# Performance work log

Hardware: AMD Instinct MI355X
Metric: run time of the kernel (lower is better)

Reference implementation:

```python
import jax, jax.numpy as jnp
import numpy as np

P, LMAX, D, H = 4096, 64, 512, 512
NEG = -1e30


def setup_inputs() -> dict:
    key = jax.random.key(0)
    ks = jax.random.split(key, 8)
    paths_nodes = jax.random.normal(ks[0], (P, LMAX, D), dtype=jnp.float32)
    lengths = jax.random.randint(ks[1], (P,), 1, LMAX + 1, dtype=jnp.int32)
    s = 0.05
    return {
        "paths_nodes": paths_nodes,
        "lengths": lengths,
        "pW1": jax.random.normal(ks[2], (D, H), dtype=jnp.float32) * s,
        "pb1": jnp.zeros((H,), dtype=jnp.float32),
        "pw2": jax.random.normal(ks[3], (H,), dtype=jnp.float32) * s,
        "pb2": jnp.zeros((1,), dtype=jnp.float32),
        "aW1": jax.random.normal(ks[4], (D, H), dtype=jnp.float32) * s,
        "ab1": jnp.zeros((H,), dtype=jnp.float32),
        "aw2": jax.random.normal(ks[5], (H,), dtype=jnp.float32) * s,
        "ab2": jnp.zeros((1,), dtype=jnp.float32),
    }


def reference(paths_nodes, lengths, pW1, pb1, pw2, pb2, aW1, ab1, aw2, ab2):
    # paths_nodes: [P, L, D], lengths: [P]
    mask = jnp.arange(LMAX)[None, :] < lengths[:, None]  # [P, L] valid positions

    # per-path node attention: Linear -> ReLU -> Linear(->1), softmax over length
    h = jax.nn.relu(jnp.einsum('pld,dh->plh', paths_nodes, pW1) + pb1)  # [P,L,H]
    scores = jnp.einsum('plh,h->pl', h, pw2) + pb2[0]                   # [P,L]
    scores = jnp.where(mask, scores, NEG)
    w = jax.nn.softmax(scores, axis=1)                                  # [P,L]
    paths_fea = jnp.einsum('pl,pld->pd', w, paths_nodes)                # [P,D]

    # path-level attention: same MLP over path features, softmax over paths
    h2 = jax.nn.relu(paths_fea @ aW1 + ab1)                             # [P,H]
    a = h2 @ aw2 + ab2[0]                                               # [P]
    aw = jax.nn.softmax(a, axis=0)                                      # [P]
    user_fea = jnp.einsum('p,pd->d', aw, paths_fea)                     # [D]
    return user_fea
```

## Files before the change

### kernel.cpp

```cpp
#include <hip/hip_runtime.h>

typedef __attribute__((ext_vector_type(8))) short bf16x8;
typedef __attribute__((ext_vector_type(8))) unsigned short u16x8;
typedef __attribute__((ext_vector_type(4))) float f32x4;

__device__ __forceinline__ ushort f2bf(float x) {
  unsigned u = __float_as_uint(x);
  unsigned r = (u + 0x7fffu + ((u >> 16) & 1u)) >> 16;
  return (ushort)r;
}

typedef const __attribute__((address_space(1))) unsigned int ga_uint;
typedef __attribute__((address_space(3))) unsigned int lds_uint;
__device__ __forceinline__ void gload_lds16(const ushort* g, ushort* l) {
  __builtin_amdgcn_global_load_lds((ga_uint*)g, (lds_uint*)l, 16, 0, 0);
}

__global__ void transpose_convert(const float* __restrict__ w1, const float* __restrict__ w2,
                                  ushort* __restrict__ o1, ushort* __restrict__ o2) {
  __shared__ float tile[64][65];
  const float* src = (blockIdx.z == 0) ? w1 : w2;
  ushort* dst = (blockIdx.z == 0) ? o1 : o2;
  const int n0 = blockIdx.x * 64, k0 = blockIdx.y * 64;
  const int tx = threadIdx.x, ty = threadIdx.y;
#pragma unroll
  for (int i = 0; i < 16; ++i) {
    int k = ty + i * 4;
    tile[k][tx] = src[(size_t)(k0 + k) * 512 + n0 + tx];
  }
  __syncthreads();
#pragma unroll
  for (int i = 0; i < 16; ++i) {
    int n = ty + i * 4;
    dst[(size_t)(n0 + n) * 512 + k0 + tx] = f2bf(tile[tx][n]);
  }
}

__global__ void convert_x(const float* __restrict__ X, const int* __restrict__ lengths,
                          ushort* __restrict__ Y) {
  const int stride = gridDim.x * blockDim.x;
  for (int i = blockIdx.x * blockDim.x + threadIdx.x; i < 16777216; i += stride) {
    const int row = i >> 6;
    const int l = row & 63, p = row >> 6;
    if (l < lengths[p]) {
      const float* s = X + (size_t)i * 8;
      float4 v0 = *(const float4*)s;
      float4 v1 = *(const float4*)(s + 4);
      u16x8 o = {f2bf(v0.x), f2bf(v0.y), f2bf(v0.z), f2bf(v0.w),
                 f2bf(v1.x), f2bf(v1.y), f2bf(v1.z), f2bf(v1.w)};
      *(u16x8*)(Y + (size_t)i * 8) = o;
    }
  }
}

__launch_bounds__(256, 3)
__global__ void gemm_score_bf16(const ushort* __restrict__ A,
                                const ushort* __restrict__ Bt,
                                const float* __restrict__ bias,
                                const float* __restrict__ wout,
                                const int* __restrict__ lengths,
                                float* __restrict__ scores) {
  __shared__ ushort As[128 * 64] __attribute__((aligned(16)));
  __shared__ ushort Bs[128 * 64] __attribute__((aligned(16)));
  __shared__ float sred[2][128];
  const int tid = threadIdx.x;
  const int wv = tid >> 6, lane = tid & 63;
  const int ln = lane & 15, quad = lane >> 4;
  const int wm = wv & 1, wn = wv >> 1;
  const int m0 = blockIdx.y * 128;
  const int nb = blockIdx.x * 128;
  const int p0 = m0 >> 6;

  const int len0 = lengths[p0], len1 = lengths[p0 + 1];
  const int mylen = wm ? len1 : len0;
  const int nms = (mylen + 15) >> 4;

  float bv[4], w2v[4];
#pragma unroll
  for (int ns = 0; ns < 4; ++ns) {
    int n = nb + wn * 64 + ns * 16 + ln;
    bv[ns] = bias[n];
    w2v[ns] = wout[n];
  }

  f32x4 acc[4][4];
  const f32x4 zero = {0.f, 0.f, 0.f, 0.f};
#pragma unroll
  for (int i = 0; i < 4; ++i)
#pragma unroll
    for (int j = 0; j < 4; ++j) acc[i][j] = zero;

  for (int kc = 0; kc < 8; ++kc) {
    const int kb = kc * 64;
    __syncthreads();
#pragma unroll
    for (int i = 0; i < 4; ++i) {
      const int id = i * 256 + tid;
      const int row = id >> 3, c = id & 7;
      const int base = (i * 256 + (tid & ~63)) * 8;
      const int r0 = i * 32 + wv * 8;
      const int rlen = (r0 < 64) ? len0 : len1;
      if ((r0 & 63) < rlen)
        gload_lds16(A + (size_t)(m0 + row) * 512 + kb + c * 8, &As[base]);
      gload_lds16(Bt + (size_t)(nb + row) * 512 + kb + c * 8, &Bs[base]);
    }
    __syncthreads();
#pragma unroll
    for (int k0 = 0; k0 < 2; ++k0) {
      bf16x8 bfr[4];
#pragma unroll
      for (int ns = 0; ns < 4; ++ns)
        bfr[ns] = *(const bf16x8*)(&Bs[(wn * 64 + ns * 16 + ln) * 64 + (quad + k0 * 4) * 8]);
#pragma unroll
      for (int ms = 0; ms < 4; ++ms) {
        if (ms < nms) {
          bf16x8 af = *(const bf16x8*)(&As[(wm * 64 + ms * 16 + ln) * 64 + (quad + k0 * 4) * 8]);
#pragma unroll
          for (int ns = 0; ns < 4; ++ns)
            acc[ms][ns] = __builtin_amdgcn_mfma_f32_16x16x32_bf16(af, bfr[ns], acc[ms][ns], 0, 0, 0);
        }
      }
    }
  }

#pragma unroll
  for (int ms = 0; ms < 4; ++ms) {
#pragma unroll
    for (int r = 0; r < 4; ++r) {
      float s = 0.f;
      if (ms < nms) {
#pragma unroll
        for (int ns = 0; ns < 4; ++ns)
          s += fmaxf(acc[ms][ns][r] + bv[ns], 0.f) * w2v[ns];
        s += __shfl_xor(s, 1);
        s += __shfl_xor(s, 2);
        s += __shfl_xor(s, 4);
        s += __shfl_xor(s, 8);
      }
      if (ln == 0) sred[wn][wm * 64 + ms * 16 + quad * 4 + r] = s;
    }
  }
  __syncthreads();
  if (tid < 128) atomicAdd(&scores[m0 + tid], sred[0][tid] + sred[1][tid]);
}

__launch_bounds__(256, 3)
__global__ void gemm_score_f32(const float* __restrict__ A,
                               const ushort* __restrict__ Bt,
                               const float* __restrict__ bias,
                               const float* __restrict__ wout,
                               float* __restrict__ scores) {
  __shared__ ushort As[128 * 64];
  __shared__ ushort Bs[128 * 64];
  __shared__ float sred[2][128];
  const int tid = threadIdx.x;
  const int wv = tid >> 6, lane = tid & 63;
  const int ln = lane & 15, quad = lane >> 4;
  const int wm = wv & 1, wn = wv >> 1;
  const int m0 = blockIdx.y * 128;
  const int nb = blockIdx.x * 128;

  float bv[4], w2v[4];
#pragma unroll
  for (int ns = 0; ns < 4; ++ns) {
    int n = nb + wn * 64 + ns * 16 + ln;
    bv[ns] = bias[n];
    w2v[ns] = wout[n];
  }

  f32x4 acc[4][4];
  const f32x4 zero = {0.f, 0.f, 0.f, 0.f};
#pragma unroll
  for (int i = 0; i < 4; ++i)
#pragma unroll
    for (int j = 0; j < 4; ++j) acc[i][j] = zero;

  int arow[4], brow[4];
#pragma unroll
  for (int ms = 0; ms < 4; ++ms) arow[ms] = wm * 64 + ms * 16 + ln;
#pragma unroll
  for (int ns = 0; ns < 4; ++ns) brow[ns] = wn * 64 + ns * 16 + ln;

  for (int kc = 0; kc < 8; ++kc) {
    const int kb = kc * 64;
    __syncthreads();
#pragma unroll
    for (int j = 0; j < 4; ++j) {
      int id = j * 256 + tid;
      int row = id >> 3, c = id & 7;
      int cs = (c ^ (row & 7)) * 8;
      const float* srcA = A + (size_t)(m0 + row) * 512 + kb + c * 8;
      float4 v0 = *(const float4*)srcA;
      float4 v1 = *(const float4*)(srcA + 4);
      u16x8 ua = {f2bf(v0.x), f2bf(v0.y), f2bf(v0.z), f2bf(v0.w),
                  f2bf(v1.x), f2bf(v1.y), f2bf(v1.z), f2bf(v1.w)};
      *(u16x8*)(&As[row * 64 + cs]) = ua;
      u16x8 ub = *(const u16x8*)(Bt + (size_t)(nb + row) * 512 + kb + c * 8);
      *(u16x8*)(&Bs[row * 64 + cs]) = ub;
    }
    __syncthreads();
#pragma unroll
    for (int k0 = 0; k0 < 2; ++k0) {
      bf16x8 af[4], bfr[4];
#pragma unroll
      for (int ms = 0; ms < 4; ++ms) {
        int r = arow[ms];
        af[ms] = *(const bf16x8*)(&As[r * 64 + (((quad + k0 * 4) ^ (r & 7)) * 8)]);
      }
#pragma unroll
      for (int ns = 0; ns < 4; ++ns) {
        int r = brow[ns];
        bfr[ns] = *(const bf16x8*)(&Bs[r * 64 + (((quad + k0 * 4) ^ (r & 7)) * 8)]);
      }
#pragma unroll
      for (int ms = 0; ms < 4; ++ms)
#pragma unroll
        for (int ns = 0; ns < 4; ++ns)
          acc[ms][ns] = __builtin_amdgcn_mfma_f32_16x16x32_bf16(af[ms], bfr[ns], acc[ms][ns], 0, 0, 0);
    }
  }

#pragma unroll
  for (int ms = 0; ms < 4; ++ms) {
#pragma unroll
    for (int r = 0; r < 4; ++r) {
      float s = 0.f;
#pragma unroll
      for (int ns = 0; ns < 4; ++ns)
        s += fmaxf(acc[ms][ns][r] + bv[ns], 0.f) * w2v[ns];
      s += __shfl_xor(s, 1);
      s += __shfl_xor(s, 2);
      s += __shfl_xor(s, 4);
      s += __shfl_xor(s, 8);
      if (ln == 0) sred[wn][wm * 64 + ms * 16 + quad * 4 + r] = s;
    }
  }
  __syncthreads();
  if (tid < 128) atomicAdd(&scores[m0 + tid], sred[0][tid] + sred[1][tid]);
}

__global__ void node_softmax(float* __restrict__ s_wl, const int* __restrict__ lengths) {
  const int p = blockIdx.x * 4 + (threadIdx.x >> 6);
  const int l = threadIdx.x & 63;
  float s = s_wl[(size_t)p * 64 + l];
  const int len = lengths[p];
  const bool valid = l < len;
  float sv = valid ? s : -1e30f;
  float mx = sv;
  mx = fmaxf(mx, __shfl_xor(mx, 1));
  mx = fmaxf(mx, __shfl_xor(mx, 2));
  mx = fmaxf(mx, __shfl_xor(mx, 4));
  mx = fmaxf(mx, __shfl_xor(mx, 8));
  mx = fmaxf(mx, __shfl_xor(mx, 16));
  mx = fmaxf(mx, __shfl_xor(mx, 32));
  float e = valid ? __expf(sv - mx) : 0.f;
  float tot = e;
  tot += __shfl_xor(tot, 1);
  tot += __shfl_xor(tot, 2);
  tot += __shfl_xor(tot, 4);
  tot += __shfl_xor(tot, 8);
  tot += __shfl_xor(tot, 16);
  tot += __shfl_xor(tot, 32);
  s_wl[(size_t)p * 64 + l] = e / tot;
}

__global__ void wsum(const float* __restrict__ X, const float* __restrict__ wl,
                     const int* __restrict__ lengths, float* __restrict__ fea) {
  __shared__ float w[64];
  const int p = blockIdx.x, tid = threadIdx.x;
  if (tid < 64) w[tid] = wl[(size_t)p * 64 + tid];
  __syncthreads();
  const int len = lengths[p];
  const float* Xp = X + (size_t)p * 32768;
  const int d0 = tid * 4;
  float4 a = {0.f, 0.f, 0.f, 0.f};
  for (int l = 0; l < len; ++l) {
    float4 x = *(const float4*)(Xp + l * 512 + d0);
    a.x = fmaf(w[l], x.x, a.x);
    a.y = fmaf(w[l], x.y, a.y);
    a.z = fmaf(w[l], x.z, a.z);
    a.w = fmaf(w[l], x.w, a.w);
  }
  *(float4*)(fea + (size_t)p * 512 + d0) = a;
}

__global__ void softmax_p(const float* __restrict__ a, float* __restrict__ aw) {
  const int tid = threadIdx.x;
  const int wv = tid >> 6;
  __shared__ float redm[4];
  __shared__ float reds[4];
  float v[16];
#pragma unroll
  for (int i = 0; i < 16; ++i) v[i] = a[i * 256 + tid];
  float mx = v[0];
#pragma unroll
  for (int i = 1; i < 16; ++i) mx = fmaxf(mx, v[i]);
  mx = fmaxf(mx, __shfl_xor(mx, 1));
  mx = fmaxf(mx, __shfl_xor(mx, 2));
  mx = fmaxf(mx, __shfl_xor(mx, 4));
  mx = fmaxf(mx, __shfl_xor(mx, 8));
  mx = fmaxf(mx, __shfl_xor(mx, 16));
  mx = fmaxf(mx, __shfl_xor(mx, 32));
  if ((tid & 63) == 0) redm[wv] = mx;
  __syncthreads();
  mx = fmaxf(fmaxf(redm[0], redm[1]), fmaxf(redm[2], redm[3]));
  float s = 0.f;
#pragma unroll
  for (int i = 0; i < 16; ++i) {
    v[i] = __expf(v[i] - mx);
    s += v[i];
  }
  s += __shfl_xor(s, 1);
  s += __shfl_xor(s, 2);
  s += __shfl_xor(s, 4);
  s += __shfl_xor(s, 8);
  s += __shfl_xor(s, 16);
  s += __shfl_xor(s, 32);
  if ((tid & 63) == 0) reds[wv] = s;
  __syncthreads();
  s = reds[0] + reds[1] + reds[2] + reds[3];
  const float inv = 1.f / s;
#pragma unroll
  for (int i = 0; i < 16; ++i) aw[i * 256 + tid] = v[i] * inv;
}

__global__ void user_accum(const float* __restrict__ fea, const float* __restrict__ aw,
                           float* __restrict__ out) {
  const int g = blockIdx.x, tid = threadIdx.x;
  const int d0 = tid * 2;
  float ax = 0.f, ay = 0.f;
  for (int p = g * 64; p < g * 64 + 64; ++p) {
    float w = aw[p];
    float2 x = *(const float2*)(fea + (size_t)p * 512 + d0);
    ax = fmaf(w, x.x, ax);
    ay = fmaf(w, x.y, ay);
  }
  atomicAdd(out + d0, ax);
  atomicAdd(out + d0 + 1, ay);
}

extern "C" void kernel_launch(void* const* d_in, const int* in_sizes, int n_in,
                              void* d_out, int out_size, void* d_ws, size_t ws_size,
                              hipStream_t stream) {
  const float* paths   = (const float*)d_in[0];
  const int*   lengths = (const int*)d_in[1];
  const float* pW1     = (const float*)d_in[2];
  const float* pb1     = (const float*)d_in[3];
  const float* pw2     = (const float*)d_in[4];
  const float* aW1     = (const float*)d_in[6];
  const float* ab1     = (const float*)d_in[7];
  const float* aw2     = (const float*)d_in[8];
  float* out = (float*)d_out;

  char* ws = (char*)d_ws;
  ushort* W1T  = (ushort*)ws;
  ushort* aW1T = (ushort*)(ws + 524288);
  float* nsc   = (float*)(ws + 1048576);
  float* fea   = (float*)(ws + 2097152);
  float* psc   = (float*)(ws + 10485760);
  float* awp   = (float*)(ws + 10502144);
  ushort* Xbf  = (ushort*)(ws + 16777216);
  const bool bf16_path = ws_size >= (16777216ull + 268435456ull);

  hipMemsetAsync(nsc, 0, 262144 * sizeof(float), stream);
  hipMemsetAsync(psc, 0, 4096 * sizeof(float), stream);
  hipMemsetAsync(d_out, 0, 512 * sizeof(float), stream);

  transpose_convert<<<dim3(8, 8, 2), dim3(64, 4), 0, stream>>>(pW1, aW1, W1T, aW1T);
  if (bf16_path) {
    convert_x<<<2048, 256, 0, stream>>>(paths, lengths, Xbf);
    gemm_score_bf16<<<dim3(4, 2048), 256, 0, stream>>>(Xbf, W1T, pb1, pw2, lengths, nsc);
  } else {
    gemm_score_f32<<<dim3(4, 2048), 256, 0, stream>>>(paths, W1T, pb1, pw2, nsc);
  }
  node_softmax<<<1024, 256, 0, stream>>>(nsc, lengths);
  wsum<<<4096, 128, 0, stream>>>(paths, nsc, lengths, fea);
  gemm_score_f32<<<dim3(4, 32), 256, 0, stream>>>(fea, aW1T, ab1, aw2, psc);
  softmax_p<<<1, 256, 0, stream>>>(psc, awp);
  user_accum<<<64, 256, 0, stream>>>(fea, awp, out);
}
```

Measured before the change: 947.9 us.

## Fuse node scoring GEMM, softmax and weighted sum into one per-path kernel

Replaces the convert_x, gemm_score_bf16, node_softmax and wsum kernels with a single kernel launched once per path. It converts fp32 X to bf16 on the fly into an XOR-swizzled LDS tile, computes all 512 hidden columns in one block, then runs the masked softmax and the weighted sum without an atomic scores buffer. This removes the separate bf16 copy of X and the score round-trips, and uses swizzling to reduce LDS bank conflicts. In exchange every block reloads the full 64 KB W1T slice per k-chunk, X is read twice from global memory, and LDS use is larger with lower occupancy (launch bounds 2).

```diff
diff --git a/kernel.cpp b/kernel.cpp
--- a/kernel.cpp
+++ b/kernel.cpp
@@ -36,88 +36,82 @@
   }
 }
 
-__global__ void convert_x(const float* __restrict__ X, const int* __restrict__ lengths,
-                          ushort* __restrict__ Y) {
-  const int stride = gridDim.x * blockDim.x;
-  for (int i = blockIdx.x * blockDim.x + threadIdx.x; i < 16777216; i += stride) {
-    const int row = i >> 6;
-    const int l = row & 63, p = row >> 6;
-    if (l < lengths[p]) {
-      const float* s = X + (size_t)i * 8;
-      float4 v0 = *(const float4*)s;
-      float4 v1 = *(const float4*)(s + 4);
-      u16x8 o = {f2bf(v0.x), f2bf(v0.y), f2bf(v0.z), f2bf(v0.w),
-                 f2bf(v1.x), f2bf(v1.y), f2bf(v1.z), f2bf(v1.w)};
-      *(u16x8*)(Y + (size_t)i * 8) = o;
-    }
-  }
-}
-
-__launch_bounds__(256, 3)
-__global__ void gemm_score_bf16(const ushort* __restrict__ A,
-                                const ushort* __restrict__ Bt,
-                                const float* __restrict__ bias,
-                                const float* __restrict__ wout,
-                                const int* __restrict__ lengths,
-                                float* __restrict__ scores) {
-  __shared__ ushort As[128 * 64] __attribute__((aligned(16)));
-  __shared__ ushort Bs[128 * 64] __attribute__((aligned(16)));
-  __shared__ float sred[2][128];
+__launch_bounds__(256, 2)
+__global__ void node_fused(const float* __restrict__ X,
+                           const int* __restrict__ lengths,
+                           const ushort* __restrict__ Bt,
+                           const float* __restrict__ bias,
+                           const float* __restrict__ wout,
+                           float* __restrict__ fea) {
+  __shared__ ushort As[64 * 64] __attribute__((aligned(16)));
+  __shared__ ushort Bs[512 * 64] __attribute__((aligned(16)));
+  __shared__ float sred[4][64];
+  __shared__ float wsm[64];
   const int tid = threadIdx.x;
   const int wv = tid >> 6, lane = tid & 63;
   const int ln = lane & 15, quad = lane >> 4;
-  const int wm = wv & 1, wn = wv >> 1;
-  const int m0 = blockIdx.y * 128;
-  const int nb = blockIdx.x * 128;
-  const int p0 = m0 >> 6;
-
-  const int len0 = lengths[p0], len1 = lengths[p0 + 1];
-  const int mylen = wm ? len1 : len0;
-  const int nms = (mylen + 15) >> 4;
-
-  float bv[4], w2v[4];
-#pragma unroll
-  for (int ns = 0; ns < 4; ++ns) {
-    int n = nb + wn * 64 + ns * 16 + ln;
+  const int p = blockIdx.x;
+  const int len = lengths[p];
+  const int nms = (len + 15) >> 4;
+  const float* Xp = X + (size_t)p * 32768;
+
+  float bv[8], w2v[8];
+#pragma unroll
+  for (int ns = 0; ns < 8; ++ns) {
+    int n = wv * 128 + ns * 16 + ln;
     bv[ns] = bias[n];
     w2v[ns] = wout[n];
   }
 
-  f32x4 acc[4][4];
+  f32x4 acc[4][8];
   const f32x4 zero = {0.f, 0.f, 0.f, 0.f};
 #pragma unroll
   for (int i = 0; i < 4; ++i)
 #pragma unroll
-    for (int j = 0; j < 4; ++j) acc[i][j] = zero;
+    for (int j = 0; j < 8; ++j) acc[i][j] = zero;
 
   for (int kc = 0; kc < 8; ++kc) {
     const int kb = kc * 64;
     __syncthreads();
 #pragma unroll
-    for (int i = 0; i < 4; ++i) {
+    for (int i = 0; i < 16; ++i) {
+      const int id = i * 256 + tid;
+      const int n = id >> 3, c = id & 7;
+      const int base = (i * 256 + (tid & ~63)) * 8;
+      gload_lds16(Bt + (size_t)n * 512 + kb + ((c ^ (n & 7)) * 8), &Bs[base]);
+    }
+#pragma unroll
+    for (int i = 0; i < 2; ++i) {
       const int id = i * 256 + tid;
       const int row = id >> 3, c = id & 7;
-      const int base = (i * 256 + (tid & ~63)) * 8;
-      const int r0 = i * 32 + wv * 8;
-      const int rlen = (r0 < 64) ? len0 : len1;
-      if ((r0 & 63) < rlen)
-        gload_lds16(A + (size_t)(m0 + row) * 512 + kb + c * 8, &As[base]);
-      gload_lds16(Bt + (size_t)(nb + row) * 512 + kb + c * 8, &Bs[base]);
+      if (row < len) {
+        const float* s = Xp + row * 512 + kb + c * 8;
+        float4 v0 = *(const float4*)s;
+        float4 v1 = *(const float4*)(s + 4);
+        u16x8 ua = {f2bf(v0.x), f2bf(v0.y), f2bf(v0.z), f2bf(v0.w),
+                    f2bf(v1.x), f2bf(v1.y), f2bf(v1.z), f2bf(v1.w)};
+        *(u16x8*)(&As[row * 64 + ((c ^ (row & 7)) * 8)]) = ua;
+      }
     }
     __syncthreads();
 #pragma unroll
     for (int k0 = 0; k0 < 2; ++k0) {
-      bf16x8 bfr[4];
-#pragma unroll
-      for (int ns = 0; ns < 4; ++ns)
-        bfr[ns] = *(const bf16x8*)(&Bs[(wn * 64 + ns * 16 + ln) * 64 + (quad + k0 * 4) * 8]);
+      bf16x8 af[4];
 #pragma unroll
       for (int ms = 0; ms < 4; ++ms) {
         if (ms < nms) {
-          bf16x8 af = *(const bf16x8*)(&As[(wm * 64 + ms * 16 + ln) * 64 + (quad + k0 * 4) * 8]);
-#pragma unroll
-          for (int ns = 0; ns < 4; ++ns)
-            acc[ms][ns] = __builtin_amdgcn_mfma_f32_16x16x32_bf16(af, bfr[ns], acc[ms][ns], 0, 0, 0);
+          int r = ms * 16 + ln;
+          af[ms] = *(const bf16x8*)(&As[r * 64 + (((quad + k0 * 4) ^ (r & 7)) * 8)]);
+        }
+      }
+#pragma unroll
+      for (int ns = 0; ns < 8; ++ns) {
+        int br = wv * 128 + ns * 16 + ln;
+        bf16x8 bfr = *(const bf16x8*)(&Bs[br * 64 + (((quad + k0 * 4) ^ (br & 7)) * 8)]);
+#pragma unroll
+        for (int ms = 0; ms < 4; ++ms) {
+          if (ms < nms)
+            acc[ms][ns] = __builtin_amdgcn_mfma_f32_16x16x32_bf16(af[ms], bfr, acc[ms][ns], 0, 0, 0);
         }
       }
     }
@@ -130,18 +124,53 @@
       float s = 0.f;
       if (ms < nms) {
 #pragma unroll
-        for (int ns = 0; ns < 4; ++ns)
+        for (int ns = 0; ns < 8; ++ns)
           s += fmaxf(acc[ms][ns][r] + bv[ns], 0.f) * w2v[ns];
         s += __shfl_xor(s, 1);
         s += __shfl_xor(s, 2);
         s += __shfl_xor(s, 4);
         s += __shfl_xor(s, 8);
       }
-      if (ln == 0) sred[wn][wm * 64 + ms * 16 + quad * 4 + r] = s;
-    }
-  }
-  __syncthreads();
-  if (tid < 128) atomicAdd(&scores[m0 + tid], sred[0][tid] + sred[1][tid]);
+      if (ln == 0) sred[wv][ms * 16 + quad * 4 + r] = s;
+    }
+  }
+  __syncthreads();
+
+  if (wv == 0) {
+    const int l = lane;
+    float s = sred[0][l] + sred[1][l] + sred[2][l] + sred[3][l];
+    const bool valid = l < len;
+    float sv = valid ? s : -1e30f;
+    float mx = sv;
+    mx = fmaxf(mx, __shfl_xor(mx, 1));
+    mx = fmaxf(mx, __shfl_xor(mx, 2));
+    mx = fmaxf(mx, __shfl_xor(mx, 4));
+    mx = fmaxf(mx, __shfl_xor(mx, 8));
+    mx = fmaxf(mx, __shfl_xor(mx, 16));
+    mx = fmaxf(mx, __shfl_xor(mx, 32));
+    float e = valid ? __expf(sv - mx) : 0.f;
+    float tot = e;
+    tot += __shfl_xor(tot, 1);
+    tot += __shfl_xor(tot, 2);
+    tot += __shfl_xor(tot, 4);
+    tot += __shfl_xor(tot, 8);
+    tot += __shfl_xor(tot, 16);
+    tot += __shfl_xor(tot, 32);
+    wsm[l] = e / tot;
+  }
+  __syncthreads();
+
+  const int d0 = tid * 2;
+  float ax = 0.f, ay = 0.f;
+#pragma unroll 4
+  for (int l = 0; l < len; ++l) {
+    float w = wsm[l];
+    float2 x = *(const float2*)(Xp + l * 512 + d0);
+    ax = fmaf(w, x.x, ax);
+    ay = fmaf(w, x.y, ay);
+  }
+  float2 o = {ax, ay};
+  *(float2*)(fea + (size_t)p * 512 + d0) = o;
 }
 
 __launch_bounds__(256, 3)
@@ -239,51 +268,6 @@
   if (tid < 128) atomicAdd(&scores[m0 + tid], sred[0][tid] + sred[1][tid]);
 }
 
-__global__ void node_softmax(float* __restrict__ s_wl, const int* __restrict__ lengths) {
-  const int p = blockIdx.x * 4 + (threadIdx.x >> 6);
-  const int l = threadIdx.x & 63;
-  float s = s_wl[(size_t)p * 64 + l];
-  const int len = lengths[p];
-  const bool valid = l < len;
-  float sv = valid ? s : -1e30f;
-  float mx = sv;
-  mx = fmaxf(mx, __shfl_xor(mx, 1));
-  mx = fmaxf(mx, __shfl_xor(mx, 2));
-  mx = fmaxf(mx, __shfl_xor(mx, 4));
-  mx = fmaxf(mx, __shfl_xor(mx, 8));
-  mx = fmaxf(mx, __shfl_xor(mx, 16));
-  mx = fmaxf(mx, __shfl_xor(mx, 32));
-  float e = valid ? __expf(sv - mx) : 0.f;
-  float tot = e;
-  tot += __shfl_xor(tot, 1);
-  tot += __shfl_xor(tot, 2);
-  tot += __shfl_xor(tot, 4);
-  tot += __shfl_xor(tot, 8);
-  tot += __shfl_xor(tot, 16);
-  tot += __shfl_xor(tot, 32);
-  s_wl[(size_t)p * 64 + l] = e / tot;
-}
-
-__global__ void wsum(const float* __restrict__ X, const float* __restrict__ wl,
-                     const int* __restrict__ lengths, float* __restrict__ fea) {
-  __shared__ float w[64];
-  const int p = blockIdx.x, tid = threadIdx.x;
-  if (tid < 64) w[tid] = wl[(size_t)p * 64 + tid];
-  __syncthreads();
-  const int len = lengths[p];
-  const float* Xp = X + (size_t)p * 32768;
-  const int d0 = tid * 4;
-  float4 a = {0.f, 0.f, 0.f, 0.f};
-  for (int l = 0; l < len; ++l) {
-    float4 x = *(const float4*)(Xp + l * 512 + d0);
-    a.x = fmaf(w[l], x.x, a.x);
-    a.y = fmaf(w[l], x.y, a.y);
-    a.z = fmaf(w[l], x.z, a.z);
-    a.w = fmaf(w[l], x.w, a.w);
-  }
-  *(float4*)(fea + (size_t)p * 512 + d0) = a;
-}
-
 __global__ void softmax_p(const float* __restrict__ a, float* __restrict__ aw) {
   const int tid = threadIdx.x;
   const int wv = tid >> 6;
@@ -355,26 +339,15 @@
   char* ws = (char*)d_ws;
   ushort* W1T  = (ushort*)ws;
   ushort* aW1T = (ushort*)(ws + 524288);
-  float* nsc   = (float*)(ws + 1048576);
   float* fea   = (float*)(ws + 2097152);
   float* psc   = (float*)(ws + 10485760);
   float* awp   = (float*)(ws + 10502144);
-  ushort* Xbf  = (ushort*)(ws + 16777216);
-  const bool bf16_path = ws_size >= (16777216ull + 268435456ull);
-
-  hipMemsetAsync(nsc, 0, 262144 * sizeof(float), stream);
+
   hipMemsetAsync(psc, 0, 4096 * sizeof(float), stream);
   hipMemsetAsync(d_out, 0, 512 * sizeof(float), stream);
 
   transpose_convert<<<dim3(8, 8, 2), dim3(64, 4), 0, stream>>>(pW1, aW1, W1T, aW1T);
-  if (bf16_path) {
-    convert_x<<<2048, 256, 0, stream>>>(paths, lengths, Xbf);
-    gemm_score_bf16<<<dim3(4, 2048), 256, 0, stream>>>(Xbf, W1T, pb1, pw2, lengths, nsc);
-  } else {
-    gemm_score_f32<<<dim3(4, 2048), 256, 0, stream>>>(paths, W1T, pb1, pw2, nsc);
-  }
-  node_softmax<<<1024, 256, 0, stream>>>(nsc, lengths);
-  wsum<<<4096, 128, 0, stream>>>(paths, nsc, lengths, fea);
+  node_fused<<<4096, 256, 0, stream>>>(paths, lengths, W1T, pb1, pw2, fea);
   gemm_score_f32<<<dim3(4, 32), 256, 0, stream>>>(fea, aW1T, ab1, aw2, psc);
   softmax_p<<<1, 256, 0, stream>>>(psc, awp);
   user_accum<<<64, 256, 0, stream>>>(fea, awp, out);
```

After: 870.8 us. 1.09x faster.
